# Performance work log

Measured on AMD Instinct MI355X. Metric: run time of the kernel, lower is better.

Reference implementation:

```python
import jax, jax.numpy as jnp
import numpy as np

B, C1, C2, H, W = 16, 64, 64, 160, 160
K, KS, HID = 4, 3, 16  # K kernels, 3x3, hidden = max(int(64/16),16)=16
EPS = 1e-5


def setup_inputs() -> dict:
    key = jax.random.key(0)
    ks = jax.random.split(key, 8)
    fan_out = KS * KS * C2
    return {
        "x": jax.random.normal(ks[0], (B, C1, H, W), jnp.float32),
        # K candidate conv kernels and biases
        "Wk": jax.random.normal(ks[1], (K, C2, C1, KS, KS), jnp.float32) * np.sqrt(2.0 / fan_out),
        "bk": jnp.zeros((K, C2), jnp.float32),
        # attention trunk: 1x1 conv C1->HID (no bias), BN, ReLU
        "Wfc": jax.random.normal(ks[2], (HID, C1), jnp.float32) * 0.1,
        "gamma_h": jnp.ones((HID,), jnp.float32),
        "beta_h": jnp.zeros((HID,), jnp.float32),
        # four attention heads
        "Wf": jax.random.normal(ks[3], (C2, HID), jnp.float32) * 0.1,
        "bf": jnp.zeros((C2,), jnp.float32),
        "Ws": jax.random.normal(ks[4], (KS * KS, HID), jnp.float32) * 0.1,
        "bs": jnp.zeros((KS * KS,), jnp.float32),
        "Wc": jax.random.normal(ks[5], (C1, HID), jnp.float32) * 0.1,
        "bc": jnp.zeros((C1,), jnp.float32),
        "Ww": jax.random.normal(ks[6], (K, HID), jnp.float32) * 0.1,
        "bw": jnp.zeros((K,), jnp.float32),
        # outer BatchNorm2d params
        "gamma_o": jnp.ones((C2,), jnp.float32),
        "beta_o": jnp.zeros((C2,), jnp.float32),
    }


def reference(x, Wk, bk, Wfc, gamma_h, beta_h, Wf, bf, Ws, bs, Wc, bc, Ww, bw, gamma_o, beta_o):
    # ---- per-sample attention over K kernels ----
    ctx = x.mean(axis=(2, 3))                      # (B, C1)  global avg pool
    h = ctx @ Wfc.T                                # (B, HID) 1x1 conv == linear
    mu = h.mean(axis=0)
    var = h.var(axis=0)                            # biased, as torch BN training
    h = (h - mu) / jnp.sqrt(var + EPS) * gamma_h + beta_h
    h = jax.nn.relu(h)
    attn_f = jax.nn.sigmoid(h @ Wf.T + bf)         # (B, C2)
    attn_s = jax.nn.sigmoid(h @ Ws.T + bs).reshape(B, KS, KS)
    attn_c = jax.nn.sigmoid(h @ Wc.T + bc)         # (B, C1)
    attn_w = jax.nn.softmax(h @ Ww.T + bw, axis=-1)  # (B, K)

    # attn: (B, K, C2, C1, KS, KS) via broadcasting
    attn = (attn_w[:, :, None, None, None, None]
            * attn_f[:, None, :, None, None, None]
            * attn_c[:, None, None, :, None, None]
            * attn_s[:, None, None, None, :, :])
    weight = jnp.sum(attn * Wk[None], axis=1)      # (B, C2, C1, KS, KS)
    bias = attn_w @ bk                             # (B, C2)

    # ---- batched conv as grouped conv with groups=B ----
    out = jax.lax.conv_general_dilated(
        x.reshape(1, B * C1, H, W),
        weight.reshape(B * C2, C1, KS, KS),
        window_strides=(1, 1), padding=((1, 1), (1, 1)),
        dimension_numbers=('NCHW', 'OIHW', 'NCHW'),
        feature_group_count=B)                     # (1, B*C2, H, W)
    out = out.reshape(B, C2, H, W) + bias[:, :, None, None]

    # ---- outer BatchNorm2d (training stats) + SiLU ----
    mu_o = out.mean(axis=(0, 2, 3))
    var_o = out.var(axis=(0, 2, 3))
    out = (out - mu_o[None, :, None, None]) / jnp.sqrt(var_o + EPS)[None, :, None, None]
    out = out * gamma_o[None, :, None, None] + beta_o[None, :, None, None]
    return out * jax.nn.sigmoid(out)               # SiLU
```

## Files before the change

### kernel.cpp

```cpp
#include <hip/hip_runtime.h>
#include <math.h>

#define BB 16
#define C1 64
#define C2 64
#define HH 160
#define WW 160
#define KK 4
#define HID 16
#define EPS 1e-5f
#define HWSZ (HH*WW)
#define NPB (BB*HWSZ)

#define WS_AF    1024
#define WS_AC    2048
#define WS_AS    3072
#define WS_AW    3216
#define WS_BIAS  3280
#define WS_SC    4304
#define WS_SH    4368
#define WS_STATS 4432
#define NSLOT    32
#define WS_PART  8704
#define WS_ZERO  49664
#define WS_WEFF  50944
#define WS_XBF   345856

typedef __attribute__((ext_vector_type(8)))  short bf16x8;
typedef __attribute__((ext_vector_type(16))) float f32x16;

__device__ __forceinline__ unsigned short f2bf(float f) {
    unsigned int u = __float_as_uint(f);
    unsigned int r = (u + 0x7FFFu + ((u >> 16) & 1u)) >> 16;
    return (unsigned short)r;
}

__device__ __forceinline__ void gload16(const void* g, void* l) {
    __builtin_amdgcn_global_load_lds(
        (const __attribute__((address_space(1))) unsigned int*)g,
        (__attribute__((address_space(3))) unsigned int*)l, 16, 0, 0);
}

__global__ __launch_bounds__(256) void xprep_kernel(const float* __restrict__ x,
                                                    float* __restrict__ ws) {
    __shared__ float lds[10240];
    int bcc = blockIdx.y;
    int rg = blockIdx.x;
    int t = threadIdx.x;

    const float* src = x + (size_t)bcc * 16 * HWSZ + (size_t)rg * 4 * WW;
    float4* l4 = (float4*)lds;
    #pragma unroll
    for (int i = 0; i < 10; ++i) {
        int g = i * 256 + t;
        int ch = g / 160, rem = g - ch * 160;
        l4[g] = *(const float4*)(src + (size_t)ch * HWSZ + rem * 4);
    }
    __syncthreads();

    {
        int ch = t >> 4, j = t & 15;
        float s = 0.f;
        #pragma unroll
        for (int m = 0; m < 40; ++m) s += lds[ch * 640 + j + 16 * m];
        #pragma unroll
        for (int o = 8; o > 0; o >>= 1) s += __shfl_down(s, o, 16);
        if (j == 0) ws[WS_PART + ((size_t)bcc * 40 + rg) * 16 + ch] = s;
    }

    uint4* dst = (uint4*)(ws + WS_XBF) + ((size_t)bcc * 160 + rg * 4) * 320;
    #pragma unroll
    for (int i = 0; i < 5; ++i) {
        int u = i * 256 + t;
        int row = u / 320, rem = u - row * 320;
        int col = rem >> 1, p = rem & 1;
        int h = p ^ ((col >> 2) & 1) ^ 1;
        union { uint4 q; unsigned short us[8]; } pk;
        #pragma unroll
        for (int k = 0; k < 8; ++k)
            pk.us[k] = f2bf(lds[(h * 8 + k) * 640 + row * 160 + col]);
        dst[u] = pk.q;
    }
}

__global__ void attn_kernel(float* __restrict__ ws,
    const float* __restrict__ Wfc, const float* __restrict__ gh, const float* __restrict__ bh,
    const float* __restrict__ Wf,  const float* __restrict__ bf,
    const float* __restrict__ Wsm, const float* __restrict__ bs,
    const float* __restrict__ Wc,  const float* __restrict__ bc,
    const float* __restrict__ Ww,  const float* __restrict__ bw,
    const float* __restrict__ bk) {
    __shared__ float ctxs[16][64];
    __shared__ float hs[16][16];
    __shared__ float aw[16][4];
    int t = threadIdx.x;

    #pragma unroll
    for (int q = 0; q < 4; ++q) {
        int idx = t * 4 + q;
        int b = idx >> 6, c1 = idx & 63;
        const float* pp = ws + WS_PART + ((size_t)(b * 4 + (c1 >> 4)) * 40) * 16 + (c1 & 15);
        float s = 0.f;
        #pragma unroll
        for (int rg = 0; rg < 40; ++rg) s += pp[rg * 16];
        ctxs[b][c1] = s * (1.0f / (float)HWSZ);
    }
    __syncthreads();
    {
        int b = t >> 4, j = t & 15;
        const float* wr = Wfc + j * 64;
        float s = 0.f;
        #pragma unroll
        for (int c = 0; c < 64; c++) s += ctxs[b][c] * wr[c];
        hs[b][j] = s;
    }
    __syncthreads();
    if (t < 16) {
        int j = t;
        float mu = 0.f;
        #pragma unroll
        for (int b = 0; b < 16; b++) mu += hs[b][j];
        mu *= (1.f / 16.f);
        float vr = 0.f;
        #pragma unroll
        for (int b = 0; b < 16; b++) { float d = hs[b][j] - mu; vr += d * d; }
        vr *= (1.f / 16.f);
        float sc = gh[j] * rsqrtf(vr + EPS);
        float sh = bh[j] - mu * sc;
        #pragma unroll
        for (int b = 0; b < 16; b++) {
            float v = hs[b][j] * sc + sh;
            hs[b][j] = v > 0.f ? v : 0.f;
        }
    }
    __syncthreads();
    if (t < 16) {
        int b = t;
        float l[4]; float mx = -1e30f;
        #pragma unroll
        for (int k = 0; k < 4; k++) {
            float s = bw[k];
            #pragma unroll
            for (int j = 0; j < 16; j++) s += hs[b][j] * Ww[k * 16 + j];
            l[k] = s; mx = fmaxf(mx, s);
        }
        float den = 0.f;
        #pragma unroll
        for (int k = 0; k < 4; k++) { l[k] = expf(l[k] - mx); den += l[k]; }
        float r = 1.f / den;
        #pragma unroll
        for (int k = 0; k < 4; k++) { float v = l[k] * r; aw[b][k] = v; ws[WS_AW + b * 4 + k] = v; }
    }
    #pragma unroll
    for (int q = 0; q < 4; q++) {
        int idx = t * 4 + q;
        int b = idx >> 6, c2 = idx & 63;
        float sf = bf[c2], sc2 = bc[c2];
        #pragma unroll
        for (int j = 0; j < 16; j++) {
            float hv = hs[b][j];
            sf  += hv * Wf[c2 * 16 + j];
            sc2 += hv * Wc[c2 * 16 + j];
        }
        ws[WS_AF + idx] = 1.f / (1.f + expf(-sf));
        ws[WS_AC + idx] = 1.f / (1.f + expf(-sc2));
    }
    if (t < 144) {
        int b = t / 9, uv = t % 9;
        float s = bs[uv];
        #pragma unroll
        for (int j = 0; j < 16; j++) s += hs[b][j] * Wsm[uv * 16 + j];
        ws[WS_AS + t] = 1.f / (1.f + expf(-s));
    }
    __syncthreads();
    #pragma unroll
    for (int q = 0; q < 4; q++) {
        int idx = t * 4 + q;
        int b = idx >> 6, c2 = idx & 63;
        float s = 0.f;
        #pragma unroll
        for (int k = 0; k < 4; k++) s += aw[b][k] * bk[k * 64 + c2];
        ws[WS_BIAS + idx] = s;
    }
    for (int i = t; i < NSLOT * 128; i += 256) ws[WS_STATS + i] = 0.f;
    for (int i = t; i < 1280; i += 256) ws[WS_ZERO + i] = 0.f;
}

__global__ void wprep_kernel(const float* __restrict__ Wk, float* __restrict__ ws) {
    int b = blockIdx.y;
    int tid = blockIdx.x * 256 + threadIdx.x;
    int h = tid & 1;
    int c2 = (tid >> 1) & 63;
    int g = tid >> 7;
    int uv = g % 9;
    int chunk = g / 9;
    const float* awp = ws + WS_AW + b * 4;
    float aw0 = awp[0], aw1 = awp[1], aw2 = awp[2], aw3 = awp[3];
    float af = ws[WS_AF + b * 64 + c2];
    float as_ = ws[WS_AS + b * 9 + uv];
    union { uint4 q; unsigned short u[8]; } pk;
    #pragma unroll
    for (int j = 0; j < 8; ++j) {
        int c1 = chunk * 16 + h * 8 + j;
        const float* wp = Wk + (size_t)(c2 * 64 + c1) * 9 + uv;
        float s = aw0 * wp[0] + aw1 * wp[64 * 64 * 9] + aw2 * wp[2 * 64 * 64 * 9] + aw3 * wp[3 * 64 * 64 * 9];
        float w = s * af * ws[WS_AC + b * 64 + c1] * as_;
        pk.u[j] = f2bf(w);
    }
    int unit = ((chunk * 9 + uv) * 64 + c2) * 2 + (h ^ ((c2 >> 2) & 1));
    ((uint4*)(ws + WS_WEFF))[(size_t)b * 4608 + unit] = pk.q;
}

__launch_bounds__(256, 2)
__global__ void conv_kernel(const float* __restrict__ wsf, float* __restrict__ out) {
    __shared__ uint4 xs[2][4 * 162 * 2];
    __shared__ uint4 wsh[2][1152];
    __shared__ float bsh[64];
    __shared__ float sst[128];

    int id = blockIdx.x;
    int b = id & 15;
    int bx = id >> 4;
    int y0 = bx * 2;
    int t = threadIdx.x;
    int wv = t >> 6;
    int lane = t & 63;
    int l31 = lane & 31;
    int l5 = lane >> 5;
    int c2h = wv & 1;
    int rw = wv >> 1;

    if (t < 64) bsh[t] = wsf[WS_BIAS + b * 64 + t];
    if (t >= 64 && t < 192) sst[t - 64] = 0.f;
    if (t >= 192 && t < 224) {
        int q = t - 192; int bq = q >> 4; q &= 15;
        int r = q >> 2, side = (q >> 1) & 1, p = q & 1;
        xs[bq][(r * 162 + side * 161) * 2 + p] = make_uint4(0, 0, 0, 0);
    }

    const uint4* weff = (const uint4*)(wsf + WS_WEFF) + (size_t)b * 4608;
    const uint4* xbf  = (const uint4*)(wsf + WS_XBF);
    const uint4* zsrc = (const uint4*)(wsf + WS_ZERO);

    auto stage = [&](int cc, int bq) {
        for (int i = wv; i < 18; i += 4)
            gload16(weff + (size_t)cc * 1152 + i * 64 + lane, (char*)&wsh[bq][0] + i * 1024);
        for (int i = wv; i < 20; i += 4) {
            int r = i / 5, seg = i % 5;
            int gy = y0 - 1 + r;
            const uint4* src = (gy >= 0 && gy < HH)
                ? xbf + (((size_t)b * 4 + cc) * 160 + gy) * 320 + seg * 64 + lane
                : zsrc + seg * 64 + lane;
            gload16(src, (char*)&xs[bq][0] + ((r * 162 + 1) * 2 + seg * 64) * 16);
        }
    };

    f32x16 acc[5];
    #pragma unroll
    for (int j = 0; j < 5; ++j)
        #pragma unroll
        for (int r = 0; r < 16; ++r) acc[j][r] = 0.f;

    stage(0, 0);

    int c2 = c2h * 32 + l31;
    int aswz = (l31 >> 2) & 1;
    int cur = 0;
    for (int cc = 0; cc < 4; ++cc) {
        if (cc < 3) {
            stage(cc + 1, cur ^ 1);
            if (wv < 2) asm volatile("s_waitcnt vmcnt(10) lgkmcnt(0)\n\ts_barrier" ::: "memory");
            else        asm volatile("s_waitcnt vmcnt(9) lgkmcnt(0)\n\ts_barrier" ::: "memory");
        } else {
            asm volatile("s_waitcnt vmcnt(0) lgkmcnt(0)\n\ts_barrier" ::: "memory");
        }

        #pragma unroll
        for (int uv = 0; uv < 9; ++uv) {
            bf16x8 a = *(bf16x8*)&wsh[cur][(uv * 64 + c2) * 2 + (l5 ^ aswz)];
            int xr = rw + uv / 3;
            int v = uv % 3;
            #pragma unroll
            for (int j = 0; j < 5; ++j) {
                int col = j * 32 + l31 + v;
                bf16x8 bb = *(bf16x8*)&xs[cur][(xr * 162 + col) * 2 + (l5 ^ (((col + 3) >> 2) & 1))];
                acc[j] = __builtin_amdgcn_mfma_f32_32x32x16_bf16(a, bb, acc[j], 0, 0, 0);
            }
        }
        asm volatile("s_barrier" ::: "memory");
        cur ^= 1;
    }

    float* outb = out + (size_t)b * C2 * HWSZ + (size_t)(y0 + rw) * WW;
    int cb = c2h * 32 + 4 * l5;
    float sr[16], qr[16];
    #pragma unroll
    for (int r = 0; r < 16; ++r) {
        int c2r = cb + (r & 3) + 8 * (r >> 2);
        float bias = bsh[c2r];
        float s = 0.f, q = 0.f;
        #pragma unroll
        for (int j = 0; j < 5; ++j) {
            float v = acc[j][r] + bias;
            outb[(size_t)c2r * HWSZ + j * 32 + l31] = v;
            s += v;
            q = fmaf(v, v, q);
        }
        sr[r] = s; qr[r] = q;
    }
    #pragma unroll
    for (int k = 0; k < 4; ++k) {
        int m = 1 << k, n = 8 >> k;
        #pragma unroll
        for (int i = 0; i < 8; ++i) {
            if (i < n) {
                float ks = (l31 & m) ? sr[i + n] : sr[i];
                float ss = (l31 & m) ? sr[i] : sr[i + n];
                sr[i] = ks + __shfl_xor(ss, m, 64);
                float kq = (l31 & m) ? qr[i + n] : qr[i];
                float sq = (l31 & m) ? qr[i] : qr[i + n];
                qr[i] = kq + __shfl_xor(sq, m, 64);
            }
        }
    }
    sr[0] += __shfl_xor(sr[0], 16, 64);
    qr[0] += __shfl_xor(qr[0], 16, 64);
    if (l31 < 16) {
        int rf = ((l31 & 1) << 3) | ((l31 & 2) << 1) | ((l31 & 4) >> 1) | ((l31 & 8) >> 3);
        int c2r = cb + (rf & 3) + 8 * (rf >> 2);
        atomicAdd(&sst[c2r], sr[0]);
        atomicAdd(&sst[64 + c2r], qr[0]);
    }
    __syncthreads();
    if (t < 128) {
        int slot = id & (NSLOT - 1);
        atomicAdd((float*)wsf + WS_STATS + slot * 128 + t, sst[t]);
    }
}

__global__ void bnstat_kernel(float* __restrict__ ws, const float* __restrict__ go,
                              const float* __restrict__ bo) {
    int c = threadIdx.x;
    float s = 0.f, q = 0.f;
    for (int sl = 0; sl < NSLOT; sl++) {
        s += ws[WS_STATS + sl * 128 + c];
        q += ws[WS_STATS + sl * 128 + 64 + c];
    }
    float mu  = s * (1.0f / (float)NPB);
    float var = q * (1.0f / (float)NPB) - mu * mu;
    float sc  = go[c] * rsqrtf(var + EPS);
    ws[WS_SC + c] = sc;
    ws[WS_SH + c] = bo[c] - mu * sc;
}

__global__ void bnact_kernel(float* __restrict__ out, const float* __restrict__ ws) {
    __shared__ float sc[64], sh[64];
    if (threadIdx.x < 64) {
        sc[threadIdx.x] = ws[WS_SC + threadIdx.x];
        sh[threadIdx.x] = ws[WS_SH + threadIdx.x];
    }
    __syncthreads();
    const int n4 = BB * C2 * HWSZ / 4;
    for (int i = blockIdx.x * blockDim.x + threadIdx.x; i < n4; i += gridDim.x * blockDim.x) {
        float4 v = ((float4*)out)[i];
        int c = ((i * 4) / HWSZ) & 63;
        float s = sc[c], h = sh[c];
        v.x = v.x * s + h; v.y = v.y * s + h; v.z = v.z * s + h; v.w = v.w * s + h;
        v.x = v.x / (1.f + __expf(-v.x));
        v.y = v.y / (1.f + __expf(-v.y));
        v.z = v.z / (1.f + __expf(-v.z));
        v.w = v.w / (1.f + __expf(-v.w));
        ((float4*)out)[i] = v;
    }
}

extern "C" void kernel_launch(void* const* d_in, const int* in_sizes, int n_in,
                              void* d_out, int out_size, void* d_ws, size_t ws_size,
                              hipStream_t stream) {
    const float* x   = (const float*)d_in[0];
    const float* Wk  = (const float*)d_in[1];
    const float* bk  = (const float*)d_in[2];
    const float* Wfc = (const float*)d_in[3];
    const float* gh  = (const float*)d_in[4];
    const float* bh  = (const float*)d_in[5];
    const float* Wf  = (const float*)d_in[6];
    const float* bf  = (const float*)d_in[7];
    const float* Wsm = (const float*)d_in[8];
    const float* bs  = (const float*)d_in[9];
    const float* Wc  = (const float*)d_in[10];
    const float* bc  = (const float*)d_in[11];
    const float* Ww  = (const float*)d_in[12];
    const float* bw  = (const float*)d_in[13];
    const float* go  = (const float*)d_in[14];
    const float* bo  = (const float*)d_in[15];
    float* out = (float*)d_out;
    float* ws  = (float*)d_ws;

    xprep_kernel<<<dim3(40, 64), dim3(256), 0, stream>>>(x, ws);
    attn_kernel<<<dim3(1), dim3(256), 0, stream>>>(ws, Wfc, gh, bh, Wf, bf, Wsm, bs, Wc, bc, Ww, bw, bk);
    wprep_kernel<<<dim3(18, 16), dim3(256), 0, stream>>>(Wk, ws);
    conv_kernel<<<dim3(1280), dim3(256), 0, stream>>>(ws, out);
    bnstat_kernel<<<dim3(1), dim3(64), 0, stream>>>(ws, go, bo);
    bnact_kernel<<<dim3(2048), dim3(256), 0, stream>>>(out, ws);
}
```

Measured before the change: 132.7 us.

## Single-buffer conv weights in LDS, zero halo rows locally, fold bnstat into bnact

The conv kernel now keeps one weight buffer in LDS instead of two. The weights for the next channel chunk are loaded only after the current MFMA loop finishes, which halves weight LDS and may allow more resident blocks. Out-of-range halo rows are zeroed directly in shared memory rather than loaded from a zero buffer in global memory. The separate single-block bnstat launch is merged into bnact, where each block recomputes the channel scale and shift. The trade-off is that weight loads are no longer overlapped with compute and each conv chunk gains an extra barrier.

```diff
diff --git a/kernel.cpp b/kernel.cpp
--- a/kernel.cpp
+++ b/kernel.cpp
@@ -183,7 +183,6 @@
         ws[WS_BIAS + idx] = s;
     }
     for (int i = t; i < NSLOT * 128; i += 256) ws[WS_STATS + i] = 0.f;
-    for (int i = t; i < 1280; i += 256) ws[WS_ZERO + i] = 0.f;
 }
 
 __global__ void wprep_kernel(const float* __restrict__ Wk, float* __restrict__ ws) {
@@ -214,7 +213,7 @@
 __launch_bounds__(256, 2)
 __global__ void conv_kernel(const float* __restrict__ wsf, float* __restrict__ out) {
     __shared__ uint4 xs[2][4 * 162 * 2];
-    __shared__ uint4 wsh[2][1152];
+    __shared__ uint4 wsh[1152];
     __shared__ float bsh[64];
     __shared__ float sst[128];
 
@@ -237,23 +236,28 @@
         int r = q >> 2, side = (q >> 1) & 1, p = q & 1;
         xs[bq][(r * 162 + side * 161) * 2 + p] = make_uint4(0, 0, 0, 0);
     }
+    int rbad = (bx == 0) ? 0 : (bx == 79 ? 3 : -1);
+    if (rbad >= 0) {
+        for (int i = t; i < 640; i += 256)
+            xs[i / 320][(rbad * 162 + 1) * 2 + (i % 320)] = make_uint4(0, 0, 0, 0);
+    }
 
     const uint4* weff = (const uint4*)(wsf + WS_WEFF) + (size_t)b * 4608;
     const uint4* xbf  = (const uint4*)(wsf + WS_XBF);
-    const uint4* zsrc = (const uint4*)(wsf + WS_ZERO);
-
-    auto stage = [&](int cc, int bq) {
-        for (int i = wv; i < 18; i += 4)
-            gload16(weff + (size_t)cc * 1152 + i * 64 + lane, (char*)&wsh[bq][0] + i * 1024);
+
+    auto stage_x = [&](int cc, int bq) {
         for (int i = wv; i < 20; i += 4) {
             int r = i / 5, seg = i % 5;
             int gy = y0 - 1 + r;
-            const uint4* src = (gy >= 0 && gy < HH)
-                ? xbf + (((size_t)b * 4 + cc) * 160 + gy) * 320 + seg * 64 + lane
-                : zsrc + seg * 64 + lane;
-            gload16(src, (char*)&xs[bq][0] + ((r * 162 + 1) * 2 + seg * 64) * 16);
+            if (gy >= 0 && gy < HH)
+                gload16(xbf + (((size_t)b * 4 + cc) * 160 + gy) * 320 + seg * 64 + lane,
+                        (char*)&xs[bq][0] + ((r * 162 + 1) * 2 + seg * 64) * 16);
         }
     };
+    auto stage_w = [&](int cc) {
+        for (int i = wv; i < 18; i += 4)
+            gload16(weff + (size_t)cc * 1152 + i * 64 + lane, (char*)wsh + i * 1024);
+    };
 
     f32x16 acc[5];
     #pragma unroll
@@ -261,23 +265,19 @@
         #pragma unroll
         for (int r = 0; r < 16; ++r) acc[j][r] = 0.f;
 
-    stage(0, 0);
+    stage_x(0, 0);
+    stage_w(0);
+    __syncthreads();
 
     int c2 = c2h * 32 + l31;
     int aswz = (l31 >> 2) & 1;
     int cur = 0;
     for (int cc = 0; cc < 4; ++cc) {
-        if (cc < 3) {
-            stage(cc + 1, cur ^ 1);
-            if (wv < 2) asm volatile("s_waitcnt vmcnt(10) lgkmcnt(0)\n\ts_barrier" ::: "memory");
-            else        asm volatile("s_waitcnt vmcnt(9) lgkmcnt(0)\n\ts_barrier" ::: "memory");
-        } else {
-            asm volatile("s_waitcnt vmcnt(0) lgkmcnt(0)\n\ts_barrier" ::: "memory");
-        }
+        if (cc < 3) stage_x(cc + 1, cur ^ 1);
 
         #pragma unroll
         for (int uv = 0; uv < 9; ++uv) {
-            bf16x8 a = *(bf16x8*)&wsh[cur][(uv * 64 + c2) * 2 + (l5 ^ aswz)];
+            bf16x8 a = *(bf16x8*)&wsh[(uv * 64 + c2) * 2 + (l5 ^ aswz)];
             int xr = rw + uv / 3;
             int v = uv % 3;
             #pragma unroll
@@ -287,7 +287,11 @@
                 acc[j] = __builtin_amdgcn_mfma_f32_32x32x16_bf16(a, bb, acc[j], 0, 0, 0);
             }
         }
-        asm volatile("s_barrier" ::: "memory");
+        asm volatile("s_waitcnt lgkmcnt(0)\n\ts_barrier" ::: "memory");
+        if (cc < 3) {
+            stage_w(cc + 1);
+            asm volatile("s_waitcnt vmcnt(0) lgkmcnt(0)\n\ts_barrier" ::: "memory");
+        }
         cur ^= 1;
     }
 
@@ -338,26 +342,22 @@
     }
 }
 
-__global__ void bnstat_kernel(float* __restrict__ ws, const float* __restrict__ go,
-                              const float* __restrict__ bo) {
-    int c = threadIdx.x;
-    float s = 0.f, q = 0.f;
-    for (int sl = 0; sl < NSLOT; sl++) {
-        s += ws[WS_STATS + sl * 128 + c];
-        q += ws[WS_STATS + sl * 128 + 64 + c];
-    }
-    float mu  = s * (1.0f / (float)NPB);
-    float var = q * (1.0f / (float)NPB) - mu * mu;
-    float sc  = go[c] * rsqrtf(var + EPS);
-    ws[WS_SC + c] = sc;
-    ws[WS_SH + c] = bo[c] - mu * sc;
-}
-
-__global__ void bnact_kernel(float* __restrict__ out, const float* __restrict__ ws) {
+__global__ void bnact_kernel(float* __restrict__ out, const float* __restrict__ ws,
+                             const float* __restrict__ go, const float* __restrict__ bo) {
     __shared__ float sc[64], sh[64];
     if (threadIdx.x < 64) {
-        sc[threadIdx.x] = ws[WS_SC + threadIdx.x];
-        sh[threadIdx.x] = ws[WS_SH + threadIdx.x];
+        int c = threadIdx.x;
+        float s = 0.f, q = 0.f;
+        #pragma unroll
+        for (int sl = 0; sl < NSLOT; sl++) {
+            s += ws[WS_STATS + sl * 128 + c];
+            q += ws[WS_STATS + sl * 128 + 64 + c];
+        }
+        float mu  = s * (1.0f / (float)NPB);
+        float var = q * (1.0f / (float)NPB) - mu * mu;
+        float scale = go[c] * rsqrtf(var + EPS);
+        sc[c] = scale;
+        sh[c] = bo[c] - mu * scale;
     }
     __syncthreads();
     const int n4 = BB * C2 * HWSZ / 4;
@@ -400,6 +400,5 @@
     attn_kernel<<<dim3(1), dim3(256), 0, stream>>>(ws, Wfc, gh, bh, Wf, bf, Wsm, bs, Wc, bc, Ww, bw, bk);
     wprep_kernel<<<dim3(18, 16), dim3(256), 0, stream>>>(Wk, ws);
     conv_kernel<<<dim3(1280), dim3(256), 0, stream>>>(ws, out);
-    bnstat_kernel<<<dim3(1), dim3(64), 0, stream>>>(ws, go, bo);
-    bnact_kernel<<<dim3(2048), dim3(256), 0, stream>>>(out, ws);
-}
+    bnact_kernel<<<dim3(2048), dim3(256), 0, stream>>>(out, ws, go, bo);
+}
```

Result: slower. 137.9 us (+3.9%).
